# Optimization experiments

Measured on AMD Instinct MI355X. Metric: run time of the kernel, lower is better.

Reference implementation:

```python
import jax, jax.numpy as jnp
import numpy as np

TEMPERATURE = 0.5  # init temperature; attn_drop=0.0 so dropout is identity


def setup_inputs() -> dict:
    key = jax.random.key(0)
    k1, k2, k3 = jax.random.split(key, 3)
    B, H, N, D = 4, 8, 2048, 64
    q = jax.random.normal(k1, (B, H, N, D), dtype=jnp.float32)
    k = jax.random.normal(k2, (B, H, N, D), dtype=jnp.float32)
    v = jax.random.normal(k3, (B, H, N, D), dtype=jnp.float32)
    scale = jnp.asarray(D ** -0.5, dtype=jnp.float32)
    return {"q": q, "k": k, "v": v, "scale": scale}


def reference(q, k, v, scale):
    # logits: [B,H,N,N]
    logits = jnp.einsum("bhqd,bhkd->bhqk", q, k) * scale
    # first softmax acts as a soft mask over keys
    soft_mask = jax.nn.softmax(logits / TEMPERATURE, axis=-1)
    # second softmax over masked logits (elementwise product, NOT matmul)
    attn = jax.nn.softmax(logits * soft_mask, axis=-1)
    # dropout with p=0.0 is identity
    out = jnp.einsum("bhqk,bhkd->bhqd", attn, v)
    return out
```

## Files before the change

### kernel.cpp

```cpp
#include <hip/hip_runtime.h>


typedef _Float16 f16;
typedef f16 f16x8 __attribute__((ext_vector_type(8)));
typedef f16 f16x4 __attribute__((ext_vector_type(4)));
typedef float f32x4 __attribute__((ext_vector_type(4)));

#define MFMA32(a, b, c) __builtin_amdgcn_mfma_f32_16x16x32_f16((a), (b), (c), 0, 0, 0)
#define MFMA16(a, b, c) __builtin_amdgcn_mfma_f32_16x16x16f16((a), (b), (c), 0, 0, 0)
#define EXP2(x) __builtin_amdgcn_exp2f(x)

#define N_CTX 2048
#define DH 64
#define KT 64
#define NKT_G 16
#define ROWS 128
#define QS 72
#define KSB (KT * QS)
#define SMEM_BYTES (4 * 2 * KSB * 2 + 2048)

#define C2 2.885390081777927f

__device__ inline unsigned pk(float a, float b) {
    typedef __fp16 fp16x2_t __attribute__((ext_vector_type(2)));
    union { fp16x2_t v; unsigned u; } x;
    x.v = __builtin_amdgcn_cvt_pkrtz(a, b);
    return x.u;
}

__global__ __launch_bounds__(256)
void stk_prep(const float* __restrict__ vg, f16* __restrict__ wsV) {
    __shared__ f16 lds[DH * QS];
    const int tid = threadIdx.x;
    const int bh = blockIdx.x >> 5, t = blockIdx.x & 31;
    const int p = tid >> 3, dseg = tid & 7, d0 = dseg * 8;
    const int c0 = ((p >> 1) & 3) * 16 + ((p >> 3) & 3) * 4 + (p & 1) * 2;
    const float* base = vg + (((size_t)(bh * 2048 + t * 64 + 2 * p)) << 6) + d0;
    float4 a0 = *(const float4*)(base);
    float4 a1 = *(const float4*)(base + 4);
    float4 b0 = *(const float4*)(base + 64);
    float4 b1 = *(const float4*)(base + 68);
    #pragma unroll
    for (int j = 0; j < 4; ++j) {
        *(unsigned*)&lds[(d0 + j) * QS + c0] =
            pk(((const float*)&a0)[j], ((const float*)&b0)[j]);
        *(unsigned*)&lds[(d0 + 4 + j) * QS + c0] =
            pk(((const float*)&a1)[j], ((const float*)&b1)[j]);
    }
    __syncthreads();
    const int d = tid >> 2, cs = tid & 3;
    f16x8 r0 = *(const f16x8*)&lds[d * QS + cs * 16];
    f16x8 r1 = *(const f16x8*)&lds[d * QS + cs * 16 + 8];
    f16* dst = wsV + ((((size_t)bh * 32 + t) << 6) + d) * 64 + cs * 16;
    *(f16x8*)(dst) = r0;
    *(f16x8*)(dst + 8) = r1;
}

__global__ __launch_bounds__(1024, 8)
void stk_attn_mfma(const float* __restrict__ qg, const float* __restrict__ kg,
                   const f16* __restrict__ wsV, const float* __restrict__ sg,
                   float* __restrict__ og) {
    extern __shared__ f16 smem[];

    const int tid  = threadIdx.x;
    const int wv   = tid >> 6;
    const int grp  = wv >> 3;
    const int wv7  = wv & 7;
    const int lane = tid & 63;
    const int l15  = lane & 15;
    const int q4   = lane >> 4;
    const int tg   = (wv7 << 6) | lane;
    const int bh   = blockIdx.x & 31;
    const int q0   = (blockIdx.x >> 5) * ROWS;
    const float scale2 = sg[0] * C2;

    const float* qb = qg + (size_t)bh * N_CTX * DH;
    float*       ob = og + (size_t)bh * N_CTX * DH;
    const float* kbg = kg + ((size_t)bh * N_CTX + grp * (NKT_G * KT)) * DH;
    const f16* wsVh = wsV + ((size_t)bh << 17);
    const int T0 = grp * NKT_G;

    f16x8 aq[2];
    {
        const float* qrow = qb + (size_t)(q0 + wv7 * 16 + l15) * DH;
        #pragma unroll
        for (int kc = 0; kc < 2; ++kc) {
            float4 a0 = *(const float4*)&qrow[kc * 32 + q4 * 8];
            float4 a1 = *(const float4*)&qrow[kc * 32 + q4 * 8 + 4];
            union { f16x8 h; unsigned u[4]; } A;
            A.u[0] = pk(a0.x * scale2, a0.y * scale2);
            A.u[1] = pk(a0.z * scale2, a0.w * scale2);
            A.u[2] = pk(a1.x * scale2, a1.y * scale2);
            A.u[3] = pk(a1.z * scale2, a1.w * scale2);
            aq[kc] = A.h;
        }
    }

    f16* const ksBase = smem + grp * (2 * KSB);
    f16* const vtBase = smem + 2 * (2 * KSB) + grp * (2 * KSB);
    float* const sred = (float*)(smem + 4 * (2 * KSB));
    float* const obuf = (float*)smem;

    int kofs[2], gofs[2];
    #pragma unroll
    for (int it = 0; it < 2; ++it) {
        int idx = it * 512 + tg;
        gofs[it] = (idx >> 4) * DH + (idx & 15) * 4;
        kofs[it] = (idx >> 4) * QS + (idx & 15) * 4;
    }
    const int sofs = tg * 8;
    const int wofs = (tg >> 3) * QS + (tg & 7) * 8;

    const f16* const ks_r = ksBase + l15 * QS + q4 * 8;
    const f16* const ksrB = vtBase + l15 * QS + q4 * 8;
    const f16* const vt_r = vtBase + l15 * QS + q4 * 16;

    float s1 = 0.f;
    float4 kra[2], krb[2];
    #pragma unroll
    for (int it = 0; it < 2; ++it) {
        kra[it] = *(const float4*)&kbg[gofs[it]];
        krb[it] = *(const float4*)&kbg[KT * DH + gofs[it]];
    }
    #pragma unroll
    for (int it = 0; it < 2; ++it) {
        *(uint2*)&ksBase[kofs[it]] =
            make_uint2(pk(kra[it].x, kra[it].y), pk(kra[it].z, kra[it].w));
        *(uint2*)&ksBase[KSB + kofs[it]] =
            make_uint2(pk(krb[it].x, krb[it].y), pk(krb[it].z, krb[it].w));
    }
    #pragma unroll
    for (int it = 0; it < 2; ++it) {
        kra[it] = *(const float4*)&kbg[2 * KT * DH + gofs[it]];
        krb[it] = *(const float4*)&kbg[3 * KT * DH + gofs[it]];
    }
    __syncthreads();

    for (int st = 0; st < 8; ++st) {
        f16* const nxtb = (st & 1) ? ksBase : vtBase;
        const f16* const crd = (st & 1) ? ksrB : ks_r;
        #pragma unroll
        for (int it = 0; it < 2; ++it) {
            *(uint2*)&nxtb[kofs[it]] =
                make_uint2(pk(kra[it].x, kra[it].y), pk(kra[it].z, kra[it].w));
            *(uint2*)&nxtb[KSB + kofs[it]] =
                make_uint2(pk(krb[it].x, krb[it].y), pk(krb[it].z, krb[it].w));
        }
        {
            int tn = (st + 2 < 8) ? st + 2 : 7;
            #pragma unroll
            for (int it = 0; it < 2; ++it) {
                kra[it] = *(const float4*)&kbg[(size_t)(2 * tn) * KT * DH + gofs[it]];
                krb[it] = *(const float4*)&kbg[(size_t)(2 * tn + 1) * KT * DH + gofs[it]];
            }
        }
        __builtin_amdgcn_s_setprio(1);
        #pragma unroll
        for (int kgi = 0; kgi < 8; ++kgi) {
            f16x8 b0 = *(const f16x8*)&crd[kgi * 16 * QS];
            f16x8 b1 = *(const f16x8*)&crd[kgi * 16 * QS + 32];
            f32x4 acc = {0.f, 0.f, 0.f, 0.f};
            acc = MFMA32(b0, aq[0], acc);
            acc = MFMA32(b1, aq[1], acc);
            s1 += (EXP2(acc[0]) + EXP2(acc[1])) + (EXP2(acc[2]) + EXP2(acc[3]));
        }
        __builtin_amdgcn_s_setprio(0);
        __syncthreads();
    }
    s1 += __shfl_xor(s1, 16, 64);
    s1 += __shfl_xor(s1, 32, 64);
    if (lane < 16) sred[(grp << 7) + (wv7 << 4) + lane] = s1;
    __syncthreads();
    s1 += sred[((grp ^ 1) << 7) + (wv7 << 4) + l15];
    const float inv1 = 0.5f / s1;

    f32x4 O[4];
    #pragma unroll
    for (int dt = 0; dt < 4; ++dt) O[dt] = (f32x4){0.f, 0.f, 0.f, 0.f};
    f32x4 Oe = {0.f, 0.f, 0.f, 0.f};
    const f16x4 ones = {(f16)1.f, (f16)1.f, (f16)1.f, (f16)1.f};

    f16* const ks_w = ksBase;
    f16* const vt_w = vtBase;
    f16x8 vrh;
    #pragma unroll
    for (int it = 0; it < 2; ++it)
        kra[it] = *(const float4*)&kbg[gofs[it]];
    vrh = *(const f16x8*)&wsVh[(size_t)T0 * 4096 + sofs];
    #pragma unroll
    for (int it = 0; it < 2; ++it)
        *(uint2*)&ks_w[kofs[it]] =
            make_uint2(pk(kra[it].x, kra[it].y), pk(kra[it].z, kra[it].w));
    *(f16x8*)&vt_w[wofs] = vrh;
    #pragma unroll
    for (int it = 0; it < 2; ++it)
        kra[it] = *(const float4*)&kbg[KT * DH + gofs[it]];
    vrh = *(const f16x8*)&wsVh[(size_t)(T0 + 1) * 4096 + sofs];
    __syncthreads();

    for (int kt = 0; kt < NKT_G; ++kt) {
        const int cur = (kt & 1) * KSB, nxt = KSB - cur;
        #pragma unroll
        for (int it = 0; it < 2; ++it)
            *(uint2*)&ks_w[nxt + kofs[it]] =
                make_uint2(pk(kra[it].x, kra[it].y), pk(kra[it].z, kra[it].w));
        *(f16x8*)&vt_w[nxt + wofs] = vrh;
        { int tn = (kt + 2 < NKT_G) ? kt + 2 : NKT_G - 1;
          #pragma unroll
          for (int it = 0; it < 2; ++it)
              kra[it] = *(const float4*)&kbg[(size_t)tn * KT * DH + gofs[it]];
          vrh = *(const f16x8*)&wsVh[(size_t)(T0 + tn) * 4096 + sofs]; }
        __builtin_amdgcn_s_setprio(1);
        #pragma unroll
        for (int p = 0; p < 2; ++p) {
            f16x4 pfr[2];
            #pragma unroll
            for (int h = 0; h < 2; ++h) {
                const int kgi = p * 2 + h;
                f16x8 b0 = *(const f16x8*)&ks_r[cur + kgi * 16 * QS];
                f16x8 b1 = *(const f16x8*)&ks_r[cur + kgi * 16 * QS + 32];
                f32x4 acc = {0.f, 0.f, 0.f, 0.f};
                acc = MFMA32(b0, aq[0], acc);
                acc = MFMA32(b1, aq[1], acc);
                float e2r[4];
                #pragma unroll
                for (int r = 0; r < 4; ++r) {
                    float a  = acc[r];
                    float e1 = EXP2(a);
                    e2r[r] = EXP2((a * e1) * inv1);
                }
                union { f16x4 hh; unsigned u[2]; } P;
                P.u[0] = pk(e2r[0], e2r[1]);
                P.u[1] = pk(e2r[2], e2r[3]);
                pfr[h] = P.hh;
                Oe = MFMA16(ones, pfr[h], Oe);
            }
            #pragma unroll
            for (int dt = 0; dt < 4; ++dt) {
                f16x8 av = *(const f16x8*)&vt_r[cur + dt * 16 * QS + p * 8];
                f16x4 alo = __builtin_shufflevector(av, av, 0, 1, 2, 3);
                f16x4 ahi = __builtin_shufflevector(av, av, 4, 5, 6, 7);
                O[dt] = MFMA16(alo, pfr[0], O[dt]);
                O[dt] = MFMA16(ahi, pfr[1], O[dt]);
            }
        }
        __builtin_amdgcn_s_setprio(0);
        __syncthreads();
    }

    const int rec = tg * 20;
    if (grp) {
        #pragma unroll
        for (int dt = 0; dt < 4; ++dt)
            *(f32x4*)&obuf[rec + dt * 4] = O[dt];
        obuf[rec + 16] = Oe[0];
    }
    __syncthreads();
    if (!grp) {
        #pragma unroll
        for (int dt = 0; dt < 4; ++dt)
            O[dt] += *(const f32x4*)&obuf[rec + dt * 4];
        const float invl2 = 1.0f / (Oe[0] + obuf[rec + 16]);
        const size_t orow = (size_t)(q0 + wv7 * 16 + l15) * DH;
        #pragma unroll
        for (int dt = 0; dt < 4; ++dt) {
            float4 o;
            o.x = O[dt][0] * invl2;
            o.y = O[dt][1] * invl2;
            o.z = O[dt][2] * invl2;
            o.w = O[dt][3] * invl2;
            *(float4*)&ob[orow + dt * 16 + q4 * 4] = o;
        }
    }
}

extern "C" void kernel_launch(void* const* d_in, const int* in_sizes, int n_in,
                              void* d_out, int out_size, void* d_ws, size_t ws_size,
                              hipStream_t stream) {
    const float* q = (const float*)d_in[0];
    const float* k = (const float*)d_in[1];
    const float* v = (const float*)d_in[2];
    const float* s = (const float*)d_in[3];
    float* out = (float*)d_out;
    f16* wsV = (f16*)d_ws;
    stk_prep<<<dim3(1024), dim3(256), 0, stream>>>(v, wsV);
    dim3 grid(32 * 16);
    stk_attn_mfma<<<grid, 1024, SMEM_BYTES, stream>>>(q, k, wsV, s, out);
}
```

Baseline: 206.6 us.

## Process two query sub-tiles per wave to reuse K/V fragments

Each wave now handles 32 query rows, as two 16-row sub-tiles, instead of 16, and the grid is halved. Every K and V fragment read from LDS feeds twice as many MFMAs, and K/V global traffic per output row is halved. The second-softmax row sum is now accumulated with VALU adds plus shuffles instead of an MFMA against a ones vector. The first pass is simplified to one tile per stage. The cost is roughly doubled accumulator register use, a lower occupancy bound (launch bounds 1024,4), and only 256 blocks, which may leave less latency hiding.

```diff
diff --git a/kernel.cpp b/kernel.cpp
--- a/kernel.cpp
+++ b/kernel.cpp
@@ -14,7 +14,6 @@
 #define DH 64
 #define KT 64
 #define NKT_G 16
-#define ROWS 128
 #define QS 72
 #define KSB (KT * QS)
 #define SMEM_BYTES (4 * 2 * KSB * 2 + 2048)
@@ -56,7 +55,7 @@
     *(f16x8*)(dst + 8) = r1;
 }
 
-__global__ __launch_bounds__(1024, 8)
+__global__ __launch_bounds__(1024, 4)
 void stk_attn_mfma(const float* __restrict__ qg, const float* __restrict__ kg,
                    const f16* __restrict__ wsV, const float* __restrict__ sg,
                    float* __restrict__ og) {
@@ -71,18 +70,19 @@
     const int q4   = lane >> 4;
     const int tg   = (wv7 << 6) | lane;
     const int bh   = blockIdx.x & 31;
-    const int q0   = (blockIdx.x >> 5) * ROWS;
+    const int q0   = (blockIdx.x >> 5) * 256;
     const float scale2 = sg[0] * C2;
 
-    const float* qb = qg + (size_t)bh * N_CTX * DH;
-    float*       ob = og + (size_t)bh * N_CTX * DH;
+    const float* qb  = qg + (size_t)bh * N_CTX * DH;
+    float*       ob  = og + (size_t)bh * N_CTX * DH;
     const float* kbg = kg + ((size_t)bh * N_CTX + grp * (NKT_G * KT)) * DH;
-    const f16* wsVh = wsV + ((size_t)bh << 17);
+    const f16* wsVh  = wsV + ((size_t)bh << 17);
     const int T0 = grp * NKT_G;
 
-    f16x8 aq[2];
-    {
-        const float* qrow = qb + (size_t)(q0 + wv7 * 16 + l15) * DH;
+    f16x8 aq[2][2];
+    #pragma unroll
+    for (int qc = 0; qc < 2; ++qc) {
+        const float* qrow = qb + (size_t)(q0 + wv7 * 32 + qc * 16 + l15) * DH;
         #pragma unroll
         for (int kc = 0; kc < 2; ++kc) {
             float4 a0 = *(const float4*)&qrow[kc * 32 + q4 * 8];
@@ -92,7 +92,7 @@
             A.u[1] = pk(a0.z * scale2, a0.w * scale2);
             A.u[2] = pk(a1.x * scale2, a1.y * scale2);
             A.u[3] = pk(a1.z * scale2, a1.w * scale2);
-            aq[kc] = A.h;
+            aq[qc][kc] = A.h;
         }
     }
 
@@ -112,89 +112,86 @@
     const int wofs = (tg >> 3) * QS + (tg & 7) * 8;
 
     const f16* const ks_r = ksBase + l15 * QS + q4 * 8;
-    const f16* const ksrB = vtBase + l15 * QS + q4 * 8;
     const f16* const vt_r = vtBase + l15 * QS + q4 * 16;
 
-    float s1 = 0.f;
-    float4 kra[2], krb[2];
-    #pragma unroll
-    for (int it = 0; it < 2; ++it) {
-        kra[it] = *(const float4*)&kbg[gofs[it]];
-        krb[it] = *(const float4*)&kbg[KT * DH + gofs[it]];
-    }
-    #pragma unroll
-    for (int it = 0; it < 2; ++it) {
+    float s1[2] = {0.f, 0.f};
+    float4 kr[2];
+    #pragma unroll
+    for (int it = 0; it < 2; ++it)
+        kr[it] = *(const float4*)&kbg[gofs[it]];
+    #pragma unroll
+    for (int it = 0; it < 2; ++it)
         *(uint2*)&ksBase[kofs[it]] =
-            make_uint2(pk(kra[it].x, kra[it].y), pk(kra[it].z, kra[it].w));
-        *(uint2*)&ksBase[KSB + kofs[it]] =
-            make_uint2(pk(krb[it].x, krb[it].y), pk(krb[it].z, krb[it].w));
-    }
-    #pragma unroll
-    for (int it = 0; it < 2; ++it) {
-        kra[it] = *(const float4*)&kbg[2 * KT * DH + gofs[it]];
-        krb[it] = *(const float4*)&kbg[3 * KT * DH + gofs[it]];
-    }
-    __syncthreads();
-
-    for (int st = 0; st < 8; ++st) {
-        f16* const nxtb = (st & 1) ? ksBase : vtBase;
-        const f16* const crd = (st & 1) ? ksrB : ks_r;
-        #pragma unroll
-        for (int it = 0; it < 2; ++it) {
-            *(uint2*)&nxtb[kofs[it]] =
-                make_uint2(pk(kra[it].x, kra[it].y), pk(kra[it].z, kra[it].w));
-            *(uint2*)&nxtb[KSB + kofs[it]] =
-                make_uint2(pk(krb[it].x, krb[it].y), pk(krb[it].z, krb[it].w));
-        }
+            make_uint2(pk(kr[it].x, kr[it].y), pk(kr[it].z, kr[it].w));
+    #pragma unroll
+    for (int it = 0; it < 2; ++it)
+        kr[it] = *(const float4*)&kbg[KT * DH + gofs[it]];
+    __syncthreads();
+
+    for (int kt = 0; kt < NKT_G; ++kt) {
+        const int cur = (kt & 1) * KSB, nxt = KSB - cur;
+        #pragma unroll
+        for (int it = 0; it < 2; ++it)
+            *(uint2*)&ksBase[nxt + kofs[it]] =
+                make_uint2(pk(kr[it].x, kr[it].y), pk(kr[it].z, kr[it].w));
         {
-            int tn = (st + 2 < 8) ? st + 2 : 7;
-            #pragma unroll
-            for (int it = 0; it < 2; ++it) {
-                kra[it] = *(const float4*)&kbg[(size_t)(2 * tn) * KT * DH + gofs[it]];
-                krb[it] = *(const float4*)&kbg[(size_t)(2 * tn + 1) * KT * DH + gofs[it]];
+            int tn = (kt + 2 < NKT_G) ? kt + 2 : NKT_G - 1;
+            #pragma unroll
+            for (int it = 0; it < 2; ++it)
+                kr[it] = *(const float4*)&kbg[(size_t)tn * KT * DH + gofs[it]];
+        }
+        __builtin_amdgcn_s_setprio(1);
+        #pragma unroll
+        for (int kgi = 0; kgi < 4; ++kgi) {
+            f16x8 b0 = *(const f16x8*)&ks_r[cur + kgi * 16 * QS];
+            f16x8 b1 = *(const f16x8*)&ks_r[cur + kgi * 16 * QS + 32];
+            #pragma unroll
+            for (int qc = 0; qc < 2; ++qc) {
+                f32x4 acc = {0.f, 0.f, 0.f, 0.f};
+                acc = MFMA32(b0, aq[qc][0], acc);
+                acc = MFMA32(b1, aq[qc][1], acc);
+                s1[qc] += (EXP2(acc[0]) + EXP2(acc[1])) + (EXP2(acc[2]) + EXP2(acc[3]));
             }
-        }
-        __builtin_amdgcn_s_setprio(1);
-        #pragma unroll
-        for (int kgi = 0; kgi < 8; ++kgi) {
-            f16x8 b0 = *(const f16x8*)&crd[kgi * 16 * QS];
-            f16x8 b1 = *(const f16x8*)&crd[kgi * 16 * QS + 32];
-            f32x4 acc = {0.f, 0.f, 0.f, 0.f};
-            acc = MFMA32(b0, aq[0], acc);
-            acc = MFMA32(b1, aq[1], acc);
-            s1 += (EXP2(acc[0]) + EXP2(acc[1])) + (EXP2(acc[2]) + EXP2(acc[3]));
         }
         __builtin_amdgcn_s_setprio(0);
         __syncthreads();
     }
-    s1 += __shfl_xor(s1, 16, 64);
-    s1 += __shfl_xor(s1, 32, 64);
-    if (lane < 16) sred[(grp << 7) + (wv7 << 4) + lane] = s1;
-    __syncthreads();
-    s1 += sred[((grp ^ 1) << 7) + (wv7 << 4) + l15];
-    const float inv1 = 0.5f / s1;
-
-    f32x4 O[4];
-    #pragma unroll
-    for (int dt = 0; dt < 4; ++dt) O[dt] = (f32x4){0.f, 0.f, 0.f, 0.f};
-    f32x4 Oe = {0.f, 0.f, 0.f, 0.f};
-    const f16x4 ones = {(f16)1.f, (f16)1.f, (f16)1.f, (f16)1.f};
-
-    f16* const ks_w = ksBase;
-    f16* const vt_w = vtBase;
+    float inv1[2];
+    #pragma unroll
+    for (int qc = 0; qc < 2; ++qc) {
+        float v = s1[qc];
+        v += __shfl_xor(v, 16, 64);
+        v += __shfl_xor(v, 32, 64);
+        s1[qc] = v;
+        if (lane < 16) sred[grp * 256 + wv7 * 32 + qc * 16 + lane] = v;
+    }
+    __syncthreads();
+    #pragma unroll
+    for (int qc = 0; qc < 2; ++qc) {
+        s1[qc] += sred[(grp ^ 1) * 256 + wv7 * 32 + qc * 16 + l15];
+        inv1[qc] = 0.5f / s1[qc];
+    }
+
+    f32x4 O[2][4];
+    #pragma unroll
+    for (int qc = 0; qc < 2; ++qc)
+        #pragma unroll
+        for (int dt = 0; dt < 4; ++dt) O[qc][dt] = (f32x4){0.f, 0.f, 0.f, 0.f};
+    float l2[2] = {0.f, 0.f};
+
     f16x8 vrh;
     #pragma unroll
     for (int it = 0; it < 2; ++it)
-        kra[it] = *(const float4*)&kbg[gofs[it]];
+        kr[it] = *(const float4*)&kbg[gofs[it]];
     vrh = *(const f16x8*)&wsVh[(size_t)T0 * 4096 + sofs];
     #pragma unroll
     for (int it = 0; it < 2; ++it)
-        *(uint2*)&ks_w[kofs[it]] =
-            make_uint2(pk(kra[it].x, kra[it].y), pk(kra[it].z, kra[it].w));
-    *(f16x8*)&vt_w[wofs] = vrh;
-    #pragma unroll
-    for (int it = 0; it < 2; ++it)
-        kra[it] = *(const float4*)&kbg[KT * DH + gofs[it]];
+        *(uint2*)&ksBase[kofs[it]] =
+            make_uint2(pk(kr[it].x, kr[it].y), pk(kr[it].z, kr[it].w));
+    *(f16x8*)&vtBase[wofs] = vrh;
+    #pragma unroll
+    for (int it = 0; it < 2; ++it)
+        kr[it] = *(const float4*)&kbg[KT * DH + gofs[it]];
     vrh = *(const f16x8*)&wsVh[(size_t)(T0 + 1) * 4096 + sofs];
     __syncthreads();
 
@@ -202,74 +199,93 @@
         const int cur = (kt & 1) * KSB, nxt = KSB - cur;
         #pragma unroll
         for (int it = 0; it < 2; ++it)
-            *(uint2*)&ks_w[nxt + kofs[it]] =
-                make_uint2(pk(kra[it].x, kra[it].y), pk(kra[it].z, kra[it].w));
-        *(f16x8*)&vt_w[nxt + wofs] = vrh;
+            *(uint2*)&ksBase[nxt + kofs[it]] =
+                make_uint2(pk(kr[it].x, kr[it].y), pk(kr[it].z, kr[it].w));
+        *(f16x8*)&vtBase[nxt + wofs] = vrh;
         { int tn = (kt + 2 < NKT_G) ? kt + 2 : NKT_G - 1;
           #pragma unroll
           for (int it = 0; it < 2; ++it)
-              kra[it] = *(const float4*)&kbg[(size_t)tn * KT * DH + gofs[it]];
+              kr[it] = *(const float4*)&kbg[(size_t)tn * KT * DH + gofs[it]];
           vrh = *(const f16x8*)&wsVh[(size_t)(T0 + tn) * 4096 + sofs]; }
         __builtin_amdgcn_s_setprio(1);
         #pragma unroll
         for (int p = 0; p < 2; ++p) {
-            f16x4 pfr[2];
+            f16x4 pfr[2][2];
             #pragma unroll
             for (int h = 0; h < 2; ++h) {
                 const int kgi = p * 2 + h;
                 f16x8 b0 = *(const f16x8*)&ks_r[cur + kgi * 16 * QS];
                 f16x8 b1 = *(const f16x8*)&ks_r[cur + kgi * 16 * QS + 32];
-                f32x4 acc = {0.f, 0.f, 0.f, 0.f};
-                acc = MFMA32(b0, aq[0], acc);
-                acc = MFMA32(b1, aq[1], acc);
-                float e2r[4];
                 #pragma unroll
-                for (int r = 0; r < 4; ++r) {
-                    float a  = acc[r];
-                    float e1 = EXP2(a);
-                    e2r[r] = EXP2((a * e1) * inv1);
+                for (int qc = 0; qc < 2; ++qc) {
+                    f32x4 acc = {0.f, 0.f, 0.f, 0.f};
+                    acc = MFMA32(b0, aq[qc][0], acc);
+                    acc = MFMA32(b1, aq[qc][1], acc);
+                    float e2r[4];
+                    #pragma unroll
+                    for (int r = 0; r < 4; ++r) {
+                        float a  = acc[r];
+                        float e1 = EXP2(a);
+                        float e2 = EXP2((a * e1) * inv1[qc]);
+                        l2[qc] += e2;
+                        e2r[r] = e2;
+                    }
+                    union { f16x4 hh; unsigned u[2]; } P;
+                    P.u[0] = pk(e2r[0], e2r[1]);
+                    P.u[1] = pk(e2r[2], e2r[3]);
+                    pfr[qc][h] = P.hh;
                 }
-                union { f16x4 hh; unsigned u[2]; } P;
-                P.u[0] = pk(e2r[0], e2r[1]);
-                P.u[1] = pk(e2r[2], e2r[3]);
-                pfr[h] = P.hh;
-                Oe = MFMA16(ones, pfr[h], Oe);
             }
             #pragma unroll
             for (int dt = 0; dt < 4; ++dt) {
                 f16x8 av = *(const f16x8*)&vt_r[cur + dt * 16 * QS + p * 8];
                 f16x4 alo = __builtin_shufflevector(av, av, 0, 1, 2, 3);
                 f16x4 ahi = __builtin_shufflevector(av, av, 4, 5, 6, 7);
-                O[dt] = MFMA16(alo, pfr[0], O[dt]);
-                O[dt] = MFMA16(ahi, pfr[1], O[dt]);
+                O[0][dt] = MFMA16(alo, pfr[0][0], O[0][dt]);
+                O[0][dt] = MFMA16(ahi, pfr[0][1], O[0][dt]);
+                O[1][dt] = MFMA16(alo, pfr[1][0], O[1][dt]);
+                O[1][dt] = MFMA16(ahi, pfr[1][1], O[1][dt]);
             }
         }
         __builtin_amdgcn_s_setprio(0);
         __syncthreads();
     }
 
-    const int rec = tg * 20;
+    #pragma unroll
+    for (int qc = 0; qc < 2; ++qc) {
+        float v = l2[qc];
+        v += __shfl_xor(v, 16, 64);
+        v += __shfl_xor(v, 32, 64);
+        l2[qc] = v;
+    }
+    const int rec = tg * 36;
     if (grp) {
         #pragma unroll
-        for (int dt = 0; dt < 4; ++dt)
-            *(f32x4*)&obuf[rec + dt * 4] = O[dt];
-        obuf[rec + 16] = Oe[0];
+        for (int qc = 0; qc < 2; ++qc)
+            #pragma unroll
+            for (int dt = 0; dt < 4; ++dt)
+                *(f32x4*)&obuf[rec + qc * 16 + dt * 4] = O[qc][dt];
+        obuf[rec + 32] = l2[0];
+        obuf[rec + 33] = l2[1];
     }
     __syncthreads();
     if (!grp) {
         #pragma unroll
-        for (int dt = 0; dt < 4; ++dt)
-            O[dt] += *(const f32x4*)&obuf[rec + dt * 4];
-        const float invl2 = 1.0f / (Oe[0] + obuf[rec + 16]);
-        const size_t orow = (size_t)(q0 + wv7 * 16 + l15) * DH;
-        #pragma unroll
-        for (int dt = 0; dt < 4; ++dt) {
-            float4 o;
-            o.x = O[dt][0] * invl2;
-            o.y = O[dt][1] * invl2;
-            o.z = O[dt][2] * invl2;
-            o.w = O[dt][3] * invl2;
-            *(float4*)&ob[orow + dt * 16 + q4 * 4] = o;
+        for (int qc = 0; qc < 2; ++qc) {
+            #pragma unroll
+            for (int dt = 0; dt < 4; ++dt)
+                O[qc][dt] += *(const f32x4*)&obuf[rec + qc * 16 + dt * 4];
+            const float invl2 = 1.0f / (l2[qc] + obuf[rec + 32 + qc]);
+            const size_t orow = (size_t)(q0 + wv7 * 32 + qc * 16 + l15) * DH;
+            #pragma unroll
+            for (int dt = 0; dt < 4; ++dt) {
+                float4 o;
+                o.x = O[qc][dt][0] * invl2;
+                o.y = O[qc][dt][1] * invl2;
+                o.z = O[qc][dt][2] * invl2;
+                o.w = O[qc][dt][3] * invl2;
+                *(float4*)&ob[orow + dt * 16 + q4 * 4] = o;
+            }
         }
     }
 }
@@ -284,6 +300,6 @@
     float* out = (float*)d_out;
     f16* wsV = (f16*)d_ws;
     stk_prep<<<dim3(1024), dim3(256), 0, stream>>>(v, wsV);
-    dim3 grid(32 * 16);
+    dim3 grid(32 * 8);
     stk_attn_mfma<<<grid, 1024, SMEM_BYTES, stream>>>(q, k, wsV, s, out);
 }
```

After: 224.1 us. +8.5%, slower.
